# Kernel optimization log

Measured on AMD Instinct MI355X. Metric: run time of the kernel, lower is better.

Reference implementation:

```python
import jax, jax.numpy as jnp
import numpy as np

B, T, E, U, V = 64, 100, 512, 512, 32000


def gru_layer(xs_tm, Wg, bg, Wc, bc):
    """TF GRUCell math. xs_tm: [T, B, D]. Returns (ys [T,B,U], h_final [B,U])."""
    u_dim = Wc.shape[1]
    h0 = jnp.zeros((xs_tm.shape[1], u_dim), xs_tm.dtype)

    def step(h, x):
        ru = jax.nn.sigmoid(jnp.concatenate([x, h], -1) @ Wg + bg)
        r, u = jnp.split(ru, 2, axis=-1)
        c = jnp.tanh(jnp.concatenate([x, r * h], -1) @ Wc + bc)
        h_new = u * h + (1.0 - u) * c
        return h_new, h_new

    h_final, ys = jax.lax.scan(step, h0, xs_tm)
    return ys, h_final


def setup_inputs() -> dict:
    key = jax.random.key(0)
    ks = jax.random.split(key, 16)

    def w(k, shape):
        fan_in = shape[0]
        return jax.random.normal(k, shape, jnp.float32) * (1.0 / np.sqrt(fan_in))

    inp = {
        "x": jax.random.randint(ks[0], (B, T), 0, V, jnp.int32),
        "embedding": jax.random.normal(ks[1], (V, E), jnp.float32) * 0.02,
        # bi-directional layer, input dim E
        "Wg_fw": w(ks[2], (E + U, 2 * U)), "bg_fw": jnp.ones((2 * U,), jnp.float32),
        "Wc_fw": w(ks[3], (E + U, U)),     "bc_fw": jnp.zeros((U,), jnp.float32),
        "Wg_bw": w(ks[4], (E + U, 2 * U)), "bg_bw": jnp.ones((2 * U,), jnp.float32),
        "Wc_bw": w(ks[5], (E + U, U)),     "bc_bw": jnp.zeros((U,), jnp.float32),
        # uni layer 1, input dim 2U (concat fw/bw)
        "Wg_u1": w(ks[6], (2 * U + U, 2 * U)), "bg_u1": jnp.ones((2 * U,), jnp.float32),
        "Wc_u1": w(ks[7], (2 * U + U, U)),     "bc_u1": jnp.zeros((U,), jnp.float32),
        # uni layer 2, input dim U
        "Wg_u2": w(ks[8], (U + U, 2 * U)), "bg_u2": jnp.ones((2 * U,), jnp.float32),
        "Wc_u2": w(ks[9], (U + U, U)),     "bc_u2": jnp.zeros((U,), jnp.float32),
    }
    return inp


def reference(x, embedding, Wg_fw, bg_fw, Wc_fw, bc_fw, Wg_bw, bg_bw, Wc_bw, bc_bw,
              Wg_u1, bg_u1, Wc_u1, bc_u1, Wg_u2, bg_u2, Wc_u2, bc_u2):
    emb = embedding[x]                      # [B, T, E] embedding lookup
    xs = jnp.swapaxes(emb, 0, 1)            # [T, B, E] time-major for scan
    # bidirectional GRU layer
    yf, _ = gru_layer(xs, Wg_fw, bg_fw, Wc_fw, bc_fw)
    yb, _ = gru_layer(xs[::-1], Wg_bw, bg_bw, Wc_bw, bc_bw)
    a = jnp.concatenate([yf, yb[::-1]], -1)  # [T, B, 2U]
    # 2-layer unidirectional GRU stack (MultiRNNCell)
    a, s1 = gru_layer(a, Wg_u1, bg_u1, Wc_u1, bc_u1)
    a, s2 = gru_layer(a, Wg_u2, bg_u2, Wc_u2, bc_u2)
    output = jnp.swapaxes(a, 0, 1)          # [B, T, U]
    state = jnp.stack([s1, s2])             # [2, B, U] per-layer final states
    return output, state
```

## Files before the change

### kernel.cpp

```cpp
#include <hip/hip_runtime.h>
#include <hip/hip_bf16.h>


#define TT 100

using f32x4 = __attribute__((ext_vector_type(4))) float;
using s16x8 = __attribute__((ext_vector_type(8))) short;
using u32x4 = __attribute__((ext_vector_type(4))) unsigned;

__device__ __forceinline__ unsigned short f2bfu(float x) {
  __hip_bfloat16 b = __float2bfloat16(x);
  unsigned short u;
  __builtin_memcpy(&u, &b, sizeof(u));
  return u;
}
__device__ __forceinline__ float bfu2f(unsigned short u) {
  __hip_bfloat16 b;
  __builtin_memcpy(&b, &u, sizeof(b));
  return __bfloat162float(b);
}
__device__ __forceinline__ float sigm(float x) {
  x = fminf(fmaxf(x, -30.f), 30.f);
  return 1.f / (1.f + __expf(-x));
}
__device__ __forceinline__ float tanh_fast(float x) {
  x = fminf(fmaxf(x, -15.f), 15.f);
  float e = __expf(-2.f * x);
  return (1.f - e) / (1.f + e);
}
__device__ __forceinline__ void vm_drain() {
  asm volatile("s_waitcnt vmcnt(0)" ::: "memory");
}
__device__ __forceinline__ void sc1_store_b16(void* p, unsigned v) {
  asm volatile("global_store_short %0, %1, off sc0 sc1" :: "v"(p), "v"(v) : "memory");
}

__global__ __launch_bounds__(256) void pack_w_kernel(const float* __restrict__ Wg,
                                                     const float* __restrict__ Wc,
                                                     int ldg, int ldc, int ktTot,
                                                     unsigned short* __restrict__ hi,
                                                     unsigned short* __restrict__ lo) {
  const int gg = blockIdx.x * 256 + threadIdx.x;
  if (gg >= 96 * ktTot * 64) return;
  const int lane = gg & 63;
  const int pair = gg >> 6;
  const int kt = pair % ktTot;
  const int nt = pair / ktTot;
  const int kg = lane >> 4;
  const int nl = lane & 15;
  const size_t off = (size_t)gg * 8;
  for (int i = 0; i < 8; ++i) {
    const int k = kt * 32 + kg * 8 + i;
    float v = (nt < 64) ? Wg[(size_t)k * ldg + nt * 16 + nl]
                        : Wc[(size_t)k * ldc + (nt - 64) * 16 + nl];
    unsigned short h = f2bfu(v);
    hi[off + i] = h;
    lo[off + i] = f2bfu(v - bfu2f(h));
  }
}

template <int ASRC>
__global__ __launch_bounds__(256) void gemm_mfma(
    const int* __restrict__ xtok, const float* __restrict__ emb,
    const unsigned short* __restrict__ aHi, const unsigned short* __restrict__ aLo, int lda,
    const unsigned short* __restrict__ bHi, const unsigned short* __restrict__ bLo,
    int ktTot, int ktX,
    const float* __restrict__ bg, const float* __restrict__ bc,
    float* __restrict__ C) {
  __shared__ unsigned short Ah[128 * 40];
  __shared__ unsigned short Al[128 * 40];

  const int tid = threadIdx.x;
  const int lane = tid & 63;
  const int w = tid >> 6;
  const int bm = blockIdx.x, bn = blockIdx.y;
  const int fm = lane & 15, fkg = lane >> 4;

  const int arow = tid >> 1;
  const int koff = (tid & 1) * 16;
  const int rowg = bm * 128 + arow;

  f32x4 acc[2][8];
#pragma unroll
  for (int rt = 0; rt < 2; ++rt)
#pragma unroll
    for (int ni = 0; ni < 8; ++ni) acc[rt][ni] = (f32x4){0.f, 0.f, 0.f, 0.f};

  for (int kt = 0; kt < ktX; ++kt) {
    __syncthreads();
    {
      const size_t so = (size_t)rowg * lda + kt * 32 + koff;
      s16x8 h0 = *(const s16x8*)(aHi + so);
      s16x8 h1 = *(const s16x8*)(aHi + so + 8);
      s16x8 l0 = *(const s16x8*)(aLo + so);
      s16x8 l1 = *(const s16x8*)(aLo + so + 8);
      *(s16x8*)(Ah + arow * 40 + koff) = h0;
      *(s16x8*)(Ah + arow * 40 + koff + 8) = h1;
      *(s16x8*)(Al + arow * 40 + koff) = l0;
      *(s16x8*)(Al + arow * 40 + koff + 8) = l1;
    }
    __syncthreads();

    s16x8 ah[2], al[2];
#pragma unroll
    for (int rt = 0; rt < 2; ++rt) {
      const int m = w * 32 + rt * 16 + fm;
      ah[rt] = *(const s16x8*)(Ah + m * 40 + fkg * 8);
      al[rt] = *(const s16x8*)(Al + m * 40 + fkg * 8);
    }
#pragma unroll
    for (int ni = 0; ni < 8; ++ni) {
      const int nt = bn * 8 + ni;
      const size_t bo = ((size_t)nt * ktTot + kt) * 512 + lane * 8;
      s16x8 bh = *(const s16x8*)(bHi + bo);
      s16x8 bl = *(const s16x8*)(bLo + bo);
#pragma unroll
      for (int rt = 0; rt < 2; ++rt) {
        acc[rt][ni] = __builtin_amdgcn_mfma_f32_16x16x32_bf16(ah[rt], bh, acc[rt][ni], 0, 0, 0);
        acc[rt][ni] = __builtin_amdgcn_mfma_f32_16x16x32_bf16(ah[rt], bl, acc[rt][ni], 0, 0, 0);
        acc[rt][ni] = __builtin_amdgcn_mfma_f32_16x16x32_bf16(al[rt], bh, acc[rt][ni], 0, 0, 0);
      }
    }
  }

#pragma unroll
  for (int ni = 0; ni < 8; ++ni) {
    const int nt = bn * 8 + ni;
    int dcol; float bias;
    if (nt < 64) { dcol = nt * 16 + fm; bias = bg[dcol]; }
    else { dcol = 1024 + (nt - 64) * 16 + fm; bias = bc[(nt - 64) * 16 + fm]; }
#pragma unroll
    for (int rt = 0; rt < 2; ++rt)
#pragma unroll
      for (int j = 0; j < 4; ++j) {
        const int row = bm * 128 + w * 32 + rt * 16 + fkg * 4 + j;
        C[(size_t)row * 1536 + dcol] = acc[rt][ni][j] + bias;
      }
  }
}

__global__ __launch_bounds__(256, 1) void bidir_scan_kernel(
    const int* __restrict__ xtok, const float* __restrict__ emb,
    const unsigned short* __restrict__ wHiF, const unsigned short* __restrict__ wLoF,
    const unsigned short* __restrict__ wHiB, const unsigned short* __restrict__ wLoB,
    const float* __restrict__ bgF, const float* __restrict__ bcF,
    const float* __restrict__ bgB, const float* __restrict__ bcB,
    unsigned* __restrict__ hPkG, unsigned* __restrict__ rPkG,
    unsigned* __restrict__ slots,
    unsigned short* __restrict__ yHi, unsigned short* __restrict__ yLo) {
  __shared__ unsigned short wHi_s[3 * 8192];
  __shared__ unsigned short wLo_s[3 * 8192];
  __shared__ float scr[4][16][17];
  __shared__ float scr2[4][16][17];
  __shared__ float scr3[4][16][17];

  const int tid = threadIdx.x;
  const int lane = tid & 63;
  const int wv = tid >> 6;
  const int bid = blockIdx.x;
  const int g = bid & 7;
  const int wg = bid >> 3;
  const int hs = wg << 4;
  const int dir = g & 1;
  const int b0 = (g >> 1) << 4;

  const unsigned short* wph = dir ? wHiB : wHiF;
  const unsigned short* wpl = dir ? wLoB : wLoF;
  const float* bgD = dir ? bgB : bgF;
  const float* bcD = dir ? bcB : bcF;

  {
    const int nt0[3] = {wg, 32 + wg, 64 + wg};
    for (int c = 0; c < 3; ++c) {
      const unsigned short* sH = wph + ((size_t)nt0[c] * 32 + 16) * 512;
      const unsigned short* sL = wpl + ((size_t)nt0[c] * 32 + 16) * 512;
      unsigned short* dH = wHi_s + c * 8192;
      unsigned short* dL = wLo_s + c * 8192;
#pragma unroll
      for (int it = 0; it < 4; ++it) {
        const int o = (it * 256 + tid) * 8;
        *(s16x8*)(dH + o) = *(const s16x8*)(sH + o);
        *(s16x8*)(dL + o) = *(const s16x8*)(sL + o);
      }
    }
  }
  __syncthreads();

  unsigned* gslots = slots + g * 32;
  const int fm = lane & 15;
  const int fkg = lane >> 4;
  const int afe = fm * 512;
  const int asw = (fm & 7) << 3;
  const int ob = tid >> 4, oj = tid & 15;
  const int ui = ob * 512 + ((hs + oj) ^ ((ob & 7) << 3));
  const size_t tileo = (size_t)g * 8192;
  const float br = bgD[hs + oj], bu = bgD[512 + hs + oj], bcv = bcD[hs + oj];

  auto mfma_regs = [&](int cidx, const s16x8* ah, const s16x8* al,
                       float (*dst)[16][17]) {
    f32x4 acc0 = {0.f, 0.f, 0.f, 0.f}, acc1 = {0.f, 0.f, 0.f, 0.f};
#pragma unroll
    for (int q = 0; q < 4; ++q) {
      const int kt = wv * 4 + q;
      const int wo = ((cidx * 16 + kt) * 64 + lane) * 8;
      s16x8 bh = *(const s16x8*)(wHi_s + wo);
      s16x8 bl = *(const s16x8*)(wLo_s + wo);
      if (q & 1) {
        acc1 = __builtin_amdgcn_mfma_f32_16x16x32_bf16(ah[q], bh, acc1, 0, 0, 0);
        acc1 = __builtin_amdgcn_mfma_f32_16x16x32_bf16(ah[q], bl, acc1, 0, 0, 0);
        acc1 = __builtin_amdgcn_mfma_f32_16x16x32_bf16(al[q], bh, acc1, 0, 0, 0);
      } else {
        acc0 = __builtin_amdgcn_mfma_f32_16x16x32_bf16(ah[q], bh, acc0, 0, 0, 0);
        acc0 = __builtin_amdgcn_mfma_f32_16x16x32_bf16(ah[q], bl, acc0, 0, 0, 0);
        acc0 = __builtin_amdgcn_mfma_f32_16x16x32_bf16(al[q], bh, acc0, 0, 0, 0);
      }
    }
#pragma unroll
    for (int j = 0; j < 4; ++j) dst[wv][fkg * 4 + j][fm] = acc0[j] + acc1[j];
  };

  auto mfma_xpg = [&](int nt, const s16x8* xh, const s16x8* xl,
                      float (*dst)[16][17]) {
    f32x4 acc0 = {0.f, 0.f, 0.f, 0.f}, acc1 = {0.f, 0.f, 0.f, 0.f};
#pragma unroll
    for (int q = 0; q < 4; ++q) {
      const int kt = wv * 4 + q;
      const size_t bo = ((size_t)nt * 32 + kt) * 512 + lane * 8;
      s16x8 bh = *(const s16x8*)(wph + bo);
      s16x8 bl = *(const s16x8*)(wpl + bo);
      if (q & 1) {
        acc1 = __builtin_amdgcn_mfma_f32_16x16x32_bf16(xh[q], bh, acc1, 0, 0, 0);
        acc1 = __builtin_amdgcn_mfma_f32_16x16x32_bf16(xh[q], bl, acc1, 0, 0, 0);
        acc1 = __builtin_amdgcn_mfma_f32_16x16x32_bf16(xl[q], bh, acc1, 0, 0, 0);
      } else {
        acc0 = __builtin_amdgcn_mfma_f32_16x16x32_bf16(xh[q], bh, acc0, 0, 0, 0);
        acc0 = __builtin_amdgcn_mfma_f32_16x16x32_bf16(xh[q], bl, acc0, 0, 0, 0);
        acc0 = __builtin_amdgcn_mfma_f32_16x16x32_bf16(xl[q], bh, acc0, 0, 0, 0);
      }
    }
#pragma unroll
    for (int j = 0; j < 4; ++j) dst[wv][fkg * 4 + j][fm] = acc0[j] + acc1[j];
  };

  auto load_emb_frags = [&](int tg, s16x8* xh, s16x8* xl) {
    const int tok = xtok[(b0 + fm) * TT + tg];
    const float* er = emb + (size_t)tok * 512;
#pragma unroll
    for (int q = 0; q < 4; ++q) {
      const int kt = wv * 4 + q;
      const float* p = er + kt * 32 + fkg * 8;
      f32x4 a = *(const f32x4*)p;
      f32x4 b = *(const f32x4*)(p + 4);
      s16x8 hh, ll;
#pragma unroll
      for (int j = 0; j < 4; ++j) {
        unsigned short h1 = f2bfu(a[j]);
        hh[j] = (short)h1; ll[j] = (short)f2bfu(a[j] - bfu2f(h1));
        unsigned short h2 = f2bfu(b[j]);
        hh[j + 4] = (short)h2; ll[j + 4] = (short)f2bfu(b[j] - bfu2f(h2));
      }
      xh[q] = hh; xl[q] = ll;
    }
  };

  auto load_frags = [&](const unsigned* pk, s16x8* ah, s16x8* al,
                        bool withHv, unsigned* hvOut) {
    u32x4 d[4][2];
#pragma unroll
    for (int q = 0; q < 4; ++q) {
      const int kt = wv * 4 + q;
      const unsigned* p = pk + tileo + afe + ((kt * 32 + fkg * 8) ^ asw);
      asm volatile("global_load_dwordx4 %0, %1, off sc0 sc1"
                   : "=v"(d[q][0]) : "v"(p) : "memory");
      asm volatile("global_load_dwordx4 %0, %1, off sc0 sc1"
                   : "=v"(d[q][1]) : "v"(p + 4) : "memory");
    }
    if (withHv)
      asm volatile("global_load_dword %0, %1, off sc0 sc1"
                   : "=v"(*hvOut) : "v"(pk + tileo + ui) : "memory");
    vm_drain();
    __builtin_amdgcn_sched_barrier(0);
#pragma unroll
    for (int q = 0; q < 4; ++q) {
      u32x4 hh, ll;
#pragma unroll
      for (int i = 0; i < 2; ++i) {
        const u32x4 dd = d[q][i];
        hh[2 * i] = (dd[0] & 0xffffu) | (dd[1] << 16);
        hh[2 * i + 1] = (dd[2] & 0xffffu) | (dd[3] << 16);
        ll[2 * i] = (dd[0] >> 16) | (dd[1] & 0xffff0000u);
        ll[2 * i + 1] = (dd[2] >> 16) | (dd[3] & 0xffff0000u);
      }
      __builtin_memcpy(&ah[q], &hh, 16);
      __builtin_memcpy(&al[q], &ll, 16);
    }
  };

  auto poll = [&](unsigned target) {
    if (tid < 32) {
      const unsigned* p = gslots + tid;
      unsigned v;
      do {
        asm volatile("global_load_dword %0, %1, off sc0 sc1\n\ts_waitcnt vmcnt(0)"
                     : "=v"(v) : "v"(p) : "memory");
      } while (!__all(v >= target));
    }
    __syncthreads();
  };

  float gxr, gxu, gxc;
  {
    s16x8 xh0[4], xl0[4];
    load_emb_frags(dir ? TT - 1 : 0, xh0, xl0);
    mfma_xpg(wg, xh0, xl0, scr);
    mfma_xpg(32 + wg, xh0, xl0, scr2);
    mfma_xpg(64 + wg, xh0, xl0, scr3);
    __syncthreads();
    gxr = scr[0][ob][oj] + scr[1][ob][oj] + scr[2][ob][oj] + scr[3][ob][oj] + br;
    gxu = scr2[0][ob][oj] + scr2[1][ob][oj] + scr2[2][ob][oj] + scr2[3][ob][oj] + bu;
    gxc = scr3[0][ob][oj] + scr3[1][ob][oj] + scr3[2][ob][oj] + scr3[3][ob][oj] + bcv;
    __syncthreads();
  }

  s16x8 xh[4], xl[4];
  for (int t = 0; t < TT; ++t) {
    const int tg = dir ? (TT - 1 - t) : t;

    s16x8 ah[4], al[4];
    unsigned hvu = 0;
    load_frags(hPkG, ah, al, true, &hvu);
    mfma_regs(0, ah, al, scr);
    __syncthreads();

    float rpre = scr[0][ob][oj] + scr[1][ob][oj] + scr[2][ob][oj] + scr[3][ob][oj] + gxr;
    float sg = sigm(rpre);
    float hv = bfu2f((unsigned short)(hvu & 0xffffu)) + bfu2f((unsigned short)(hvu >> 16));
    float rh = sg * hv;
    {
      unsigned short hh_ = f2bfu(rh);
      unsigned short ll_ = f2bfu(rh - bfu2f(hh_));
      unsigned e = (unsigned)hh_ | ((unsigned)ll_ << 16);
      asm volatile("global_store_dword %0, %1, off sc0 sc1"
                   :: "v"(rPkG + tileo + ui), "v"(e) : "memory");
    }
    vm_drain();
    __syncthreads();
    if (tid == 0) {
      unsigned tv = 2 * t + 1;
      asm volatile("global_store_dword %0, %1, off sc0 sc1"
                   :: "v"(gslots + wg), "v"(tv) : "memory");
    }

    mfma_regs(1, ah, al, scr2);
    float ngxr = 0.f, ngxu = 0.f, ngxc = 0.f;
    if (t + 1 < TT) {
      load_emb_frags(dir ? TT - 2 - t : t + 1, xh, xl);
      mfma_xpg(32 + wg, xh, xl, scr);
      mfma_xpg(64 + wg, xh, xl, scr3);
      __syncthreads();
      ngxu = scr[0][ob][oj] + scr[1][ob][oj] + scr[2][ob][oj] + scr[3][ob][oj] + bu;
      ngxc = scr3[0][ob][oj] + scr3[1][ob][oj] + scr3[2][ob][oj] + scr3[3][ob][oj] + bcv;
      __syncthreads();
    }

    poll(2 * t + 1);

    load_frags(rPkG, ah, al, false, nullptr);
    mfma_regs(2, ah, al, scr);
    __syncthreads();

    float upre = scr2[0][ob][oj] + scr2[1][ob][oj] + scr2[2][ob][oj] + scr2[3][ob][oj] + gxu;
    float uv = sigm(upre);
    float cpre = scr[0][ob][oj] + scr[1][ob][oj] + scr[2][ob][oj] + scr[3][ob][oj] + gxc;
    float hn = uv * hv + (1.f - uv) * tanh_fast(cpre);
    unsigned short hh_ = f2bfu(hn);
    unsigned short ll_ = f2bfu(hn - bfu2f(hh_));

    if (t == TT - 1) {
      const size_t yi = ((size_t)tg * 64 + (b0 + ob)) * 1024 + dir * 512 + hs + oj;
      yHi[yi] = hh_; yLo[yi] = ll_;
      break;
    }

    {
      unsigned e = (unsigned)hh_ | ((unsigned)ll_ << 16);
      asm volatile("global_store_dword %0, %1, off sc0 sc1"
                   :: "v"(hPkG + tileo + ui), "v"(e) : "memory");
    }
    vm_drain();
    __syncthreads();
    if (tid == 0) {
      unsigned tv = 2 * t + 2;
      asm volatile("global_store_dword %0, %1, off sc0 sc1"
                   :: "v"(gslots + wg), "v"(tv) : "memory");
    }

    {
      const size_t yi = ((size_t)tg * 64 + (b0 + ob)) * 1024 + dir * 512 + hs + oj;
      yHi[yi] = hh_; yLo[yi] = ll_;
    }
    {
      mfma_xpg(wg, xh, xl, scr);
      __syncthreads();
      ngxr = scr[0][ob][oj] + scr[1][ob][oj] + scr[2][ob][oj] + scr[3][ob][oj] + br;
    }
    gxr = ngxr; gxu = ngxu; gxc = ngxc;

    poll(2 * t + 2);
  }
}

__global__ __launch_bounds__(256, 1) void uni_fused_kernel(
    const float* __restrict__ gx1,
    const unsigned short* __restrict__ w1Hi, const unsigned short* __restrict__ w1Lo,
    const unsigned short* __restrict__ w2Hi, const unsigned short* __restrict__ w2Lo,
    const float* __restrict__ bg2, const float* __restrict__ bc2,
    unsigned* __restrict__ hPk1, unsigned* __restrict__ rPk1,
    unsigned* __restrict__ hPk2, unsigned* __restrict__ rPk2,
    unsigned* __restrict__ slots1, unsigned* __restrict__ slots2,
    unsigned short* __restrict__ y1Hi, unsigned short* __restrict__ y1Lo,
    float* __restrict__ out, float* __restrict__ st1, float* __restrict__ st2) {
  __shared__ unsigned short wHi_s[3 * 8192];
  __shared__ unsigned short wLo_s[3 * 8192];
  __shared__ float scr[4][16][17];
  __shared__ float scr2[4][16][17];
  __shared__ float scr3[4][16][17];

  const int tid = threadIdx.x;
  const int lane = tid & 63;
  const int wv = tid >> 6;
  const int bid = blockIdx.x;
  const int role = (bid >= 128);
  const int g = (bid & 127) >> 5;
  const int wg = bid & 31;
  const int hs = wg << 4;
  const int b0 = g * 16;

  const unsigned short* wph = role ? w2Hi : w1Hi;
  const unsigned short* wpl = role ? w2Lo : w1Lo;
  const int ktTot = role ? 32 : 48;
  const int ktH0 = role ? 16 : 32;
  unsigned* hPk = role ? hPk2 : hPk1;
  unsigned* rPk = role ? rPk2 : rPk1;
  unsigned* myslots = (role ? slots2 : slots1) + g * 32;
  unsigned* u1gs = slots1 + g * 32;

  {
    const int nt0[3] = {wg, 32 + wg, 64 + wg};
    for (int c = 0; c < 3; ++c) {
      const unsigned short* sH = wph + ((size_t)nt0[c] * ktTot + ktH0) * 512;
      const unsigned short* sL = wpl + ((size_t)nt0[c] * ktTot + ktH0) * 512;
      unsigned short* dH = wHi_s + c * 8192;
      unsigned short* dL = wLo_s + c * 8192;
#pragma unroll
      for (int it = 0; it < 4; ++it) {
        const int o = (it * 256 + tid) * 8;
        *(s16x8*)(dH + o) = *(const s16x8*)(sH + o);
        *(s16x8*)(dL + o) = *(const s16x8*)(sL + o);
      }
    }
  }
  __syncthreads();

  const int fm = lane & 15;
  const int fkg = lane >> 4;
  const int afe = fm * 512;
  const int asw = (fm & 7) << 3;
  const int ob = tid >> 4, oj = tid & 15;
  const int ui = ob * 512 + ((hs + oj) ^ ((ob & 7) << 3));
  const size_t tileo = (size_t)g * 8192;

  auto mfma_regs = [&](int cidx, const s16x8* ah, const s16x8* al,
                       float (*dst)[16][17]) {
    f32x4 acc0 = {0.f, 0.f, 0.f, 0.f}, acc1 = {0.f, 0.f, 0.f, 0.f};
#pragma unroll
    for (int q = 0; q < 4; ++q) {
      const int kt = wv * 4 + q;
      const int wo = ((cidx * 16 + kt) * 64 + lane) * 8;
      s16x8 bh = *(const s16x8*)(wHi_s + wo);
      s16x8 bl = *(const s16x8*)(wLo_s + wo);
      if (q & 1) {
        acc1 = __builtin_amdgcn_mfma_f32_16x16x32_bf16(ah[q], bh, acc1, 0, 0, 0);
        acc1 = __builtin_amdgcn_mfma_f32_16x16x32_bf16(ah[q], bl, acc1, 0, 0, 0);
        acc1 = __builtin_amdgcn_mfma_f32_16x16x32_bf16(al[q], bh, acc1, 0, 0, 0);
      } else {
        acc0 = __builtin_amdgcn_mfma_f32_16x16x32_bf16(ah[q], bh, acc0, 0, 0, 0);
        acc0 = __builtin_amdgcn_mfma_f32_16x16x32_bf16(ah[q], bl, acc0, 0, 0, 0);
        acc0 = __builtin_amdgcn_mfma_f32_16x16x32_bf16(al[q], bh, acc0, 0, 0, 0);
      }
    }
#pragma unroll
    for (int j = 0; j < 4; ++j) dst[wv][fkg * 4 + j][fm] = acc0[j] + acc1[j];
  };

  auto mfma_xp = [&](int cidx, const s16x8* xh, const s16x8* xl,
                     float (*dst)[16][17]) {
    const int nt0[3] = {wg, 32 + wg, 64 + wg};
    f32x4 acc0 = {0.f, 0.f, 0.f, 0.f}, acc1 = {0.f, 0.f, 0.f, 0.f};
#pragma unroll
    for (int q = 0; q < 4; ++q) {
      const int kt = wv * 4 + q;
      const size_t bo = ((size_t)nt0[cidx] * 32 + kt) * 512 + lane * 8;
      s16x8 bh = *(const s16x8*)(w2Hi + bo);
      s16x8 bl = *(const s16x8*)(w2Lo + bo);
      if (q & 1) {
        acc1 = __builtin_amdgcn_mfma_f32_16x16x32_bf16(xh[q], bh, acc1, 0, 0, 0);
        acc1 = __builtin_amdgcn_mfma_f32_16x16x32_bf16(xh[q], bl, acc1, 0, 0, 0);
        acc1 = __builtin_amdgcn_mfma_f32_16x16x32_bf16(xl[q], bh, acc1, 0, 0, 0);
      } else {
        acc0 = __builtin_amdgcn_mfma_f32_16x16x32_bf16(xh[q], bh, acc0, 0, 0, 0);
        acc0 = __builtin_amdgcn_mfma_f32_16x16x32_bf16(xh[q], bl, acc0, 0, 0, 0);
        acc0 = __builtin_amdgcn_mfma_f32_16x16x32_bf16(xl[q], bh, acc0, 0, 0, 0);
      }
    }
#pragma unroll
    for (int j = 0; j < 4; ++j) dst[wv][fkg * 4 + j][fm] = acc0[j] + acc1[j];
  };

  auto load_y1_frags = [&](int t_, s16x8* xh, s16x8* xl) {
#pragma unroll
    for (int q = 0; q < 4; ++q) {
      const int kt = wv * 4 + q;
      const size_t yo = ((size_t)t_ * 64 + b0 + fm) * 512 + kt * 32 + fkg * 8;
      asm volatile("global_load_dwordx4 %0, %1, off sc0 sc1"
                   : "=v"(xh[q]) : "v"(y1Hi + yo) : "memory");
      asm volatile("global_load_dwordx4 %0, %1, off sc0 sc1"
                   : "=v"(xl[q]) : "v"(y1Lo + yo) : "memory");
    }
    vm_drain();
    __builtin_amdgcn_sched_barrier(0);
  };

  auto load_frags = [&](const unsigned* pk, s16x8* ah, s16x8* al,
                        bool withHv, unsigned* hvOut) {
    u32x4 d[4][2];
#pragma unroll
    for (int q = 0; q < 4; ++q) {
      const int kt = wv * 4 + q;
      const unsigned* p = pk + tileo + afe + ((kt * 32 + fkg * 8) ^ asw);
      asm volatile("global_load_dwordx4 %0, %1, off sc0 sc1"
                   : "=v"(d[q][0]) : "v"(p) : "memory");
      asm volatile("global_load_dwordx4 %0, %1, off sc0 sc1"
                   : "=v"(d[q][1]) : "v"(p + 4) : "memory");
    }
    if (withHv)
      asm volatile("global_load_dword %0, %1, off sc0 sc1"
                   : "=v"(*hvOut) : "v"(pk + tileo + ui) : "memory");
    vm_drain();
    __builtin_amdgcn_sched_barrier(0);
#pragma unroll
    for (int q = 0; q < 4; ++q) {
      u32x4 hh, ll;
#pragma unroll
      for (int i = 0; i < 2; ++i) {
        const u32x4 dd = d[q][i];
        hh[2 * i] = (dd[0] & 0xffffu) | (dd[1] << 16);
        hh[2 * i + 1] = (dd[2] & 0xffffu) | (dd[3] << 16);
        ll[2 * i] = (dd[0] >> 16) | (dd[1] & 0xffff0000u);
        ll[2 * i + 1] = (dd[2] >> 16) | (dd[3] & 0xffff0000u);
      }
      __builtin_memcpy(&ah[q], &hh, 16);
      __builtin_memcpy(&al[q], &ll, 16);
    }
  };

  auto poll_arr = [&](const unsigned* arr, unsigned target) {
    if (tid < 32) {
      const unsigned* p = arr + tid;
      unsigned v;
      do {
        asm volatile("global_load_dword %0, %1, off sc0 sc1\n\ts_waitcnt vmcnt(0)"
                     : "=v"(v) : "v"(p) : "memory");
      } while (!__all(v >= target));
    }
    __syncthreads();
  };

  if (role == 0) {
    float gxr, gxu, gxc;
    {
      const float* row = gx1 + ((size_t)0 * 64 + b0 + ob) * 1536 + hs + oj;
      gxr = row[0]; gxu = row[512]; gxc = row[1024];
    }
    for (int t = 0; t < TT; ++t) {
      s16x8 ah[4], al[4];
      unsigned hvu = 0;
      load_frags(hPk, ah, al, true, &hvu);
      mfma_regs(0, ah, al, scr);
      __syncthreads();

      float rpre = scr[0][ob][oj] + scr[1][ob][oj] + scr[2][ob][oj] + scr[3][ob][oj] + gxr;
      float sg = sigm(rpre);
      float hv = bfu2f((unsigned short)(hvu & 0xffffu)) + bfu2f((unsigned short)(hvu >> 16));
      float rh = sg * hv;
      {
        unsigned short hh_ = f2bfu(rh);
        unsigned short ll_ = f2bfu(rh - bfu2f(hh_));
        unsigned e = (unsigned)hh_ | ((unsigned)ll_ << 16);
        asm volatile("global_store_dword %0, %1, off sc0 sc1"
                     :: "v"(rPk + tileo + ui), "v"(e) : "memory");
      }
      vm_drain();
      __syncthreads();
      if (tid == 0) {
        unsigned tv = 2 * t + 1;
        asm volatile("global_store_dword %0, %1, off sc0 sc1"
                     :: "v"(myslots + wg), "v"(tv) : "memory");
      }

      mfma_regs(1, ah, al, scr2);

      float ngxr = 0.f, ngxu = 0.f, ngxc = 0.f;
      if (t + 1 < TT) {
        const float* row = gx1 + ((size_t)(t + 1) * 64 + b0 + ob) * 1536 + hs + oj;
        ngxr = row[0]; ngxu = row[512]; ngxc = row[1024];
      }

      poll_arr(myslots, 2 * t + 1);

      load_frags(rPk, ah, al, false, nullptr);
      mfma_regs(2, ah, al, scr);
      __syncthreads();

      float upre = scr2[0][ob][oj] + scr2[1][ob][oj] + scr2[2][ob][oj] + scr2[3][ob][oj] + gxu;
      float uv = sigm(upre);
      float cpre = scr[0][ob][oj] + scr[1][ob][oj] + scr[2][ob][oj] + scr[3][ob][oj] + gxc;
      float hn = uv * hv + (1.f - uv) * tanh_fast(cpre);
      unsigned short hh_ = f2bfu(hn);
      unsigned short ll_ = f2bfu(hn - bfu2f(hh_));

      {
        const size_t yi = ((size_t)t * 64 + (b0 + ob)) * 512 + hs + oj;
        sc1_store_b16(y1Hi + yi, hh_);
        sc1_store_b16(y1Lo + yi, ll_);
      }
      if (t < TT - 1) {
        unsigned e = (unsigned)hh_ | ((unsigned)ll_ << 16);
        asm volatile("global_store_dword %0, %1, off sc0 sc1"
                     :: "v"(hPk + tileo + ui), "v"(e) : "memory");
      } else {
        st1[(size_t)(b0 + ob) * 512 + hs + oj] = hn;
      }
      vm_drain();
      __syncthreads();
      if (tid == 0) {
        unsigned tv = 2 * t + 2;
        asm volatile("global_store_dword %0, %1, off sc0 sc1"
                     :: "v"(myslots + wg), "v"(tv) : "memory");
      }
      if (t == TT - 1) break;
      gxr = ngxr; gxu = ngxu; gxc = ngxc;
      poll_arr(myslots, 2 * t + 2);
    }
  } else {
    const float br = bg2[hs + oj], bu = bg2[512 + hs + oj], bc_ = bc2[hs + oj];
    s16x8 xh[4], xl[4];
    float gxr, gxu, gxc;
    {
      poll_arr(u1gs, 2);
      load_y1_frags(0, xh, xl);
      mfma_xp(0, xh, xl, scr);
      mfma_xp(1, xh, xl, scr2);
      mfma_xp(2, xh, xl, scr3);
      __syncthreads();
      gxr = scr[0][ob][oj] + scr[1][ob][oj] + scr[2][ob][oj] + scr[3][ob][oj] + br;
      gxu = scr2[0][ob][oj] + scr2[1][ob][oj] + scr2[2][ob][oj] + scr2[3][ob][oj] + bu;
      gxc = scr3[0][ob][oj] + scr3[1][ob][oj] + scr3[2][ob][oj] + scr3[3][ob][oj] + bc_;
      __syncthreads();
    }
    for (int t = 0; t < TT; ++t) {
      s16x8 ah[4], al[4];
      unsigned hvu = 0;
      load_frags(hPk, ah, al, true, &hvu);
      mfma_regs(0, ah, al, scr);
      __syncthreads();

      float rpre = scr[0][ob][oj] + scr[1][ob][oj] + scr[2][ob][oj] + scr[3][ob][oj] + gxr;
      float sg = sigm(rpre);
      float hv = bfu2f((unsigned short)(hvu & 0xffffu)) + bfu2f((unsigned short)(hvu >> 16));
      float rh = sg * hv;
      {
        unsigned short hh_ = f2bfu(rh);
        unsigned short ll_ = f2bfu(rh - bfu2f(hh_));
        unsigned e = (unsigned)hh_ | ((unsigned)ll_ << 16);
        asm volatile("global_store_dword %0, %1, off sc0 sc1"
                     :: "v"(rPk + tileo + ui), "v"(e) : "memory");
      }
      vm_drain();
      __syncthreads();
      if (tid == 0) {
        unsigned tv = 2 * t + 1;
        asm volatile("global_store_dword %0, %1, off sc0 sc1"
                     :: "v"(myslots + wg), "v"(tv) : "memory");
      }

      mfma_regs(1, ah, al, scr2);
      float ngxr = 0.f, ngxu = 0.f, ngxc = 0.f;
      if (t + 1 < TT) {
        poll_arr(u1gs, 2 * (t + 1) + 2);
        load_y1_frags(t + 1, xh, xl);
        mfma_xp(1, xh, xl, scr);
        mfma_xp(2, xh, xl, scr3);
        __syncthreads();
        ngxu = scr[0][ob][oj] + scr[1][ob][oj] + scr[2][ob][oj] + scr[3][ob][oj] + bu;
        ngxc = scr3[0][ob][oj] + scr3[1][ob][oj] + scr3[2][ob][oj] + scr3[3][ob][oj] + bc_;
        __syncthreads();
      }

      poll_arr(myslots, 2 * t + 1);

      load_frags(rPk, ah, al, false, nullptr);
      mfma_regs(2, ah, al, scr);
      __syncthreads();

      float upre = scr2[0][ob][oj] + scr2[1][ob][oj] + scr2[2][ob][oj] + scr2[3][ob][oj] + gxu;
      float uv = sigm(upre);
      float cpre = scr[0][ob][oj] + scr[1][ob][oj] + scr[2][ob][oj] + scr[3][ob][oj] + gxc;
      float hn = uv * hv + (1.f - uv) * tanh_fast(cpre);

      if (t == TT - 1) {
        out[((size_t)(b0 + ob) * TT + t) * 512 + hs + oj] = hn;
        st2[(size_t)(b0 + ob) * 512 + hs + oj] = hn;
        break;
      }
      {
        unsigned short hh_ = f2bfu(hn);
        unsigned short ll_ = f2bfu(hn - bfu2f(hh_));
        unsigned e = (unsigned)hh_ | ((unsigned)ll_ << 16);
        asm volatile("global_store_dword %0, %1, off sc0 sc1"
                     :: "v"(hPk + tileo + ui), "v"(e) : "memory");
      }
      vm_drain();
      __syncthreads();
      if (tid == 0) {
        unsigned tv = 2 * t + 2;
        asm volatile("global_store_dword %0, %1, off sc0 sc1"
                     :: "v"(myslots + wg), "v"(tv) : "memory");
      }

      out[((size_t)(b0 + ob) * TT + t) * 512 + hs + oj] = hn;
      {
        mfma_xp(0, xh, xl, scr);
        __syncthreads();
        ngxr = scr[0][ob][oj] + scr[1][ob][oj] + scr[2][ob][oj] + scr[3][ob][oj] + br;
      }
      gxr = ngxr; gxu = ngxu; gxc = ngxc;
      poll_arr(myslots, 2 * t + 2);
    }
  }
}

extern "C" void kernel_launch(void* const* d_in, const int* in_sizes, int n_in,
                              void* d_out, int out_size, void* d_ws, size_t ws_size,
                              hipStream_t stream) {
  (void)in_sizes; (void)n_in; (void)out_size; (void)ws_size;
  const int* x = (const int*)d_in[0];
  const float* emb = (const float*)d_in[1];
  const float* WgFw = (const float*)d_in[2];
  const float* bgFw = (const float*)d_in[3];
  const float* WcFw = (const float*)d_in[4];
  const float* bcFw = (const float*)d_in[5];
  const float* WgBw = (const float*)d_in[6];
  const float* bgBw = (const float*)d_in[7];
  const float* WcBw = (const float*)d_in[8];
  const float* bcBw = (const float*)d_in[9];
  const float* WgU1 = (const float*)d_in[10];
  const float* bgU1 = (const float*)d_in[11];
  const float* WcU1 = (const float*)d_in[12];
  const float* bcU1 = (const float*)d_in[13];
  const float* WgU2 = (const float*)d_in[14];
  const float* bgU2 = (const float*)d_in[15];
  const float* WcU2 = (const float*)d_in[16];
  const float* bcU2 = (const float*)d_in[17];

  char* ws = (char*)d_ws;
  float* bufA = (float*)(ws + 0);
  unsigned short* ycatHi = (unsigned short*)(ws + 78643200);
  unsigned short* ycatLo = (unsigned short*)(ws + 91750400);
  unsigned short* y1Hi = (unsigned short*)(ws + 78643200);
  unsigned short* y1Lo = (unsigned short*)(ws + 85196800);
  unsigned short* wpFwHi = (unsigned short*)(ws + 104857600);
  unsigned short* wpFwLo = (unsigned short*)(ws + 108003328);
  unsigned short* wpBwHi = (unsigned short*)(ws + 111149056);
  unsigned short* wpBwLo = (unsigned short*)(ws + 114294784);
  unsigned short* wpU1Hi = (unsigned short*)(ws + 117440512);
  unsigned short* wpU1Lo = (unsigned short*)(ws + 122159104);
  unsigned short* wpU2Hi = (unsigned short*)(ws + 104857600);
  unsigned short* wpU2Lo = (unsigned short*)(ws + 108003328);
  unsigned* tiles = (unsigned*)(ws + 126877696);
  unsigned* bars = (unsigned*)(ws + 127401984);

  unsigned* hPkB = tiles;
  unsigned* rPkB = tiles + 65536;
  unsigned* hPk1 = tiles;
  unsigned* rPk1 = tiles + 32768;
  unsigned* hPk2 = tiles + 65536;
  unsigned* rPk2 = tiles + 98304;

  float* out = (float*)d_out;
  float* st1 = out + (size_t)64 * TT * 512;
  float* st2 = st1 + 64 * 512;

  hipMemsetAsync(bars, 0, 4096, stream);

  pack_w_kernel<<<768, 256, 0, stream>>>(WgFw, WcFw, 1024, 512, 32, wpFwHi, wpFwLo);
  pack_w_kernel<<<768, 256, 0, stream>>>(WgBw, WcBw, 1024, 512, 32, wpBwHi, wpBwLo);
  pack_w_kernel<<<1152, 256, 0, stream>>>(WgU1, WcU1, 1024, 512, 48, wpU1Hi, wpU1Lo);

  hipMemsetAsync(tiles, 0, 524288, stream);
  {
    const int* xt = x;
    const float* em = emb;
    const unsigned short *w0 = wpFwHi, *w1 = wpFwLo, *w2 = wpBwHi, *w3 = wpBwLo;
    const float *bF = bgFw, *cF = bcFw, *bB = bgBw, *cB = bcBw;
    unsigned *h0 = hPkB, *r0 = rPkB;
    unsigned* bp = bars;
    unsigned short *yh = ycatHi, *yl = ycatLo;
    void* args[] = {&xt, &em, &w0, &w1, &w2, &w3, &bF, &cF, &bB, &cB,
                    &h0, &r0, &bp, &yh, &yl};
    hipLaunchCooperativeKernel((const void*)bidir_scan_kernel, dim3(256), dim3(256),
                               args, 0, stream);
  }

  pack_w_kernel<<<768, 256, 0, stream>>>(WgU2, WcU2, 1024, 512, 32, wpU2Hi, wpU2Lo);

  gemm_mfma<1><<<dim3(50, 12), 256, 0, stream>>>(
      nullptr, nullptr, ycatHi, ycatLo, 1024, wpU1Hi, wpU1Lo, 48, 32, bgU1, bcU1, bufA);

  hipMemsetAsync(tiles, 0, 524288, stream);
  {
    const float* a0 = bufA;
    const unsigned short *w0 = wpU1Hi, *w1 = wpU1Lo, *w2 = wpU2Hi, *w3 = wpU2Lo;
    const float *b2 = bgU2, *c2 = bcU2;
    unsigned *h1 = hPk1, *r1 = rPk1, *h2 = hPk2, *r2 = rPk2;
    unsigned *s1p = bars + 256, *s2p = bars + 384;
    unsigned short *yh = y1Hi, *yl = y1Lo;
    float *op = out, *t1 = st1, *t2 = st2;
    void* args[] = {&a0, &w0, &w1, &w2, &w3, &b2, &c2,
                    &h1, &r1, &h2, &r2, &s1p, &s2p, &yh, &yl, &op, &t1, &t2};
    hipLaunchCooperativeKernel((const void*)uni_fused_kernel, dim3(256), dim3(256),
                               args, 0, stream);
  }
}
```

Baseline: 1.555 ms.

## Replace slot-counter barriers with tagged data records and double-buffered state tiles

Inter-block synchronization in the recurrent scan kernels no longer uses per-group counter slots with drain, syncthreads and polling. Each hidden-state and r*h value is now stored as a 64-bit record carrying its timestep tag, and consumers spin until every record they load has the expected tag. The h tiles are double-buffered by timestep parity so writers never overwrite data still being read. The goal is to remove the store-drain, flag-write and poll round trips from the critical path of each step. The cost is doubled payload traffic for state loads, a larger memset including a 26 MB y1 record buffer, and retry loads when data is not yet ready.

```diff
diff --git a/kernel.cpp b/kernel.cpp
--- a/kernel.cpp
+++ b/kernel.cpp
@@ -6,7 +6,11 @@
 
 using f32x4 = __attribute__((ext_vector_type(4))) float;
 using s16x8 = __attribute__((ext_vector_type(8))) short;
+using u32x2 = __attribute__((ext_vector_type(2))) unsigned;
 using u32x4 = __attribute__((ext_vector_type(4))) unsigned;
+typedef unsigned long long u64;
+
+#define PARSTRIDE 65536
 
 __device__ __forceinline__ unsigned short f2bfu(float x) {
   __hip_bfloat16 b = __float2bfloat16(x);
@@ -31,8 +35,9 @@
 __device__ __forceinline__ void vm_drain() {
   asm volatile("s_waitcnt vmcnt(0)" ::: "memory");
 }
-__device__ __forceinline__ void sc1_store_b16(void* p, unsigned v) {
-  asm volatile("global_store_short %0, %1, off sc0 sc1" :: "v"(p), "v"(v) : "memory");
+__device__ __forceinline__ void rec_store(u64* p, unsigned val, unsigned tag) {
+  u32x2 e; e[0] = val; e[1] = tag;
+  asm volatile("global_store_dwordx2 %0, %1, off sc0 sc1" :: "v"(p), "v"(e) : "memory");
 }
 
 __global__ __launch_bounds__(256) void pack_w_kernel(const float* __restrict__ Wg,
@@ -59,9 +64,7 @@
   }
 }
 
-template <int ASRC>
 __global__ __launch_bounds__(256) void gemm_mfma(
-    const int* __restrict__ xtok, const float* __restrict__ emb,
     const unsigned short* __restrict__ aHi, const unsigned short* __restrict__ aLo, int lda,
     const unsigned short* __restrict__ bHi, const unsigned short* __restrict__ bLo,
     int ktTot, int ktX,
@@ -145,14 +148,16 @@
     const unsigned short* __restrict__ wHiB, const unsigned short* __restrict__ wLoB,
     const float* __restrict__ bgF, const float* __restrict__ bcF,
     const float* __restrict__ bgB, const float* __restrict__ bcB,
-    unsigned* __restrict__ hPkG, unsigned* __restrict__ rPkG,
-    unsigned* __restrict__ slots,
+    u64* __restrict__ hT0, u64* __restrict__ rT0,
     unsigned short* __restrict__ yHi, unsigned short* __restrict__ yLo) {
   __shared__ unsigned short wHi_s[3 * 8192];
   __shared__ unsigned short wLo_s[3 * 8192];
-  __shared__ float scr[4][16][17];
-  __shared__ float scr2[4][16][17];
-  __shared__ float scr3[4][16][17];
+  __shared__ float scrR[4][16][17];
+  __shared__ float scrU[4][16][17];
+  __shared__ float scrC[4][16][17];
+  __shared__ float scrXU[4][16][17];
+  __shared__ float scrXC[4][16][17];
+  __shared__ float scrXR[4][16][17];
 
   const int tid = threadIdx.x;
   const int lane = tid & 63;
@@ -186,7 +191,6 @@
   }
   __syncthreads();
 
-  unsigned* gslots = slots + g * 32;
   const int fm = lane & 15;
   const int fkg = lane >> 4;
   const int afe = fm * 512;
@@ -263,150 +267,125 @@
     }
   };
 
-  auto load_frags = [&](const unsigned* pk, s16x8* ah, s16x8* al,
-                        bool withHv, unsigned* hvOut) {
-    u32x4 d[4][2];
+  auto load_frags_tag = [&](const u64* pkt, unsigned tag, s16x8* ah, s16x8* al,
+                            bool withHv, unsigned* hvOut) {
+    u32x4 d[4][4];
+    u32x2 hv2 = {0, 0};
+    while (true) {
+#pragma unroll
+      for (int q = 0; q < 4; ++q) {
+        const int kt = wv * 4 + q;
+        const unsigned* p = (const unsigned*)(pkt + tileo + afe + ((kt * 32 + fkg * 8) ^ asw));
+#pragma unroll
+        for (int i = 0; i < 4; ++i)
+          asm volatile("global_load_dwordx4 %0, %1, off sc0 sc1"
+                       : "=v"(d[q][i]) : "v"(p + 4 * i) : "memory");
+      }
+      if (withHv)
+        asm volatile("global_load_dwordx2 %0, %1, off sc0 sc1"
+                     : "=v"(hv2) : "v"((const unsigned*)(pkt + tileo + ui)) : "memory");
+      vm_drain();
+      __builtin_amdgcn_sched_barrier(0);
+      bool ok = true;
+#pragma unroll
+      for (int q = 0; q < 4; ++q)
+#pragma unroll
+        for (int i = 0; i < 4; ++i) ok &= (d[q][i][1] == tag) & (d[q][i][3] == tag);
+      if (withHv) ok &= (hv2[1] == tag);
+      if (__all(ok)) break;
+      __builtin_amdgcn_s_sleep(1);
+    }
+    if (withHv) *hvOut = hv2[0];
 #pragma unroll
     for (int q = 0; q < 4; ++q) {
-      const int kt = wv * 4 + q;
-      const unsigned* p = pk + tileo + afe + ((kt * 32 + fkg * 8) ^ asw);
-      asm volatile("global_load_dwordx4 %0, %1, off sc0 sc1"
-                   : "=v"(d[q][0]) : "v"(p) : "memory");
-      asm volatile("global_load_dwordx4 %0, %1, off sc0 sc1"
-                   : "=v"(d[q][1]) : "v"(p + 4) : "memory");
-    }
-    if (withHv)
-      asm volatile("global_load_dword %0, %1, off sc0 sc1"
-                   : "=v"(*hvOut) : "v"(pk + tileo + ui) : "memory");
-    vm_drain();
-    __builtin_amdgcn_sched_barrier(0);
-#pragma unroll
-    for (int q = 0; q < 4; ++q) {
+      unsigned val[8];
+#pragma unroll
+      for (int j = 0; j < 8; ++j) val[j] = d[q][j >> 1][(j & 1) * 2];
       u32x4 hh, ll;
 #pragma unroll
-      for (int i = 0; i < 2; ++i) {
-        const u32x4 dd = d[q][i];
-        hh[2 * i] = (dd[0] & 0xffffu) | (dd[1] << 16);
-        hh[2 * i + 1] = (dd[2] & 0xffffu) | (dd[3] << 16);
-        ll[2 * i] = (dd[0] >> 16) | (dd[1] & 0xffff0000u);
-        ll[2 * i + 1] = (dd[2] >> 16) | (dd[3] & 0xffff0000u);
+      for (int k = 0; k < 4; ++k) {
+        const unsigned v0 = val[2 * k], v1 = val[2 * k + 1];
+        hh[k] = (v0 & 0xffffu) | (v1 << 16);
+        ll[k] = (v0 >> 16) | (v1 & 0xffff0000u);
       }
       __builtin_memcpy(&ah[q], &hh, 16);
       __builtin_memcpy(&al[q], &ll, 16);
     }
-  };
-
-  auto poll = [&](unsigned target) {
-    if (tid < 32) {
-      const unsigned* p = gslots + tid;
-      unsigned v;
-      do {
-        asm volatile("global_load_dword %0, %1, off sc0 sc1\n\ts_waitcnt vmcnt(0)"
-                     : "=v"(v) : "v"(p) : "memory");
-      } while (!__all(v >= target));
-    }
-    __syncthreads();
   };
 
   float gxr, gxu, gxc;
   {
     s16x8 xh0[4], xl0[4];
     load_emb_frags(dir ? TT - 1 : 0, xh0, xl0);
-    mfma_xpg(wg, xh0, xl0, scr);
-    mfma_xpg(32 + wg, xh0, xl0, scr2);
-    mfma_xpg(64 + wg, xh0, xl0, scr3);
-    __syncthreads();
-    gxr = scr[0][ob][oj] + scr[1][ob][oj] + scr[2][ob][oj] + scr[3][ob][oj] + br;
-    gxu = scr2[0][ob][oj] + scr2[1][ob][oj] + scr2[2][ob][oj] + scr2[3][ob][oj] + bu;
-    gxc = scr3[0][ob][oj] + scr3[1][ob][oj] + scr3[2][ob][oj] + scr3[3][ob][oj] + bcv;
+    mfma_xpg(wg, xh0, xl0, scrR);
+    mfma_xpg(32 + wg, xh0, xl0, scrU);
+    mfma_xpg(64 + wg, xh0, xl0, scrC);
+    __syncthreads();
+    gxr = scrR[0][ob][oj] + scrR[1][ob][oj] + scrR[2][ob][oj] + scrR[3][ob][oj] + br;
+    gxu = scrU[0][ob][oj] + scrU[1][ob][oj] + scrU[2][ob][oj] + scrU[3][ob][oj] + bu;
+    gxc = scrC[0][ob][oj] + scrC[1][ob][oj] + scrC[2][ob][oj] + scrC[3][ob][oj] + bcv;
     __syncthreads();
   }
 
   s16x8 xh[4], xl[4];
   for (int t = 0; t < TT; ++t) {
     const int tg = dir ? (TT - 1 - t) : t;
+    u64* hTc = hT0 + (size_t)(t & 1) * PARSTRIDE;
+    u64* hTn = hT0 + (size_t)((t + 1) & 1) * PARSTRIDE;
+    u64* rTc = rT0 + (size_t)(t & 1) * PARSTRIDE;
 
     s16x8 ah[4], al[4];
     unsigned hvu = 0;
-    load_frags(hPkG, ah, al, true, &hvu);
-    mfma_regs(0, ah, al, scr);
-    __syncthreads();
-
-    float rpre = scr[0][ob][oj] + scr[1][ob][oj] + scr[2][ob][oj] + scr[3][ob][oj] + gxr;
+    load_frags_tag(hTc, (unsigned)t, ah, al, true, &hvu);
+    mfma_regs(0, ah, al, scrR);
+    __syncthreads();
+
+    float rpre = scrR[0][ob][oj] + scrR[1][ob][oj] + scrR[2][ob][oj] + scrR[3][ob][oj] + gxr;
     float sg = sigm(rpre);
     float hv = bfu2f((unsigned short)(hvu & 0xffffu)) + bfu2f((unsigned short)(hvu >> 16));
     float rh = sg * hv;
     {
       unsigned short hh_ = f2bfu(rh);
       unsigned short ll_ = f2bfu(rh - bfu2f(hh_));
-      unsigned e = (unsigned)hh_ | ((unsigned)ll_ << 16);
-      asm volatile("global_store_dword %0, %1, off sc0 sc1"
-                   :: "v"(rPkG + tileo + ui), "v"(e) : "memory");
-    }
-    vm_drain();
-    __syncthreads();
-    if (tid == 0) {
-      unsigned tv = 2 * t + 1;
-      asm volatile("global_store_dword %0, %1, off sc0 sc1"
-                   :: "v"(gslots + wg), "v"(tv) : "memory");
-    }
-
-    mfma_regs(1, ah, al, scr2);
+      rec_store(rTc + tileo + ui, (unsigned)hh_ | ((unsigned)ll_ << 16), (unsigned)(t + 1));
+    }
+
+    mfma_regs(1, ah, al, scrU);
     float ngxr = 0.f, ngxu = 0.f, ngxc = 0.f;
     if (t + 1 < TT) {
       load_emb_frags(dir ? TT - 2 - t : t + 1, xh, xl);
-      mfma_xpg(32 + wg, xh, xl, scr);
-      mfma_xpg(64 + wg, xh, xl, scr3);
-      __syncthreads();
-      ngxu = scr[0][ob][oj] + scr[1][ob][oj] + scr[2][ob][oj] + scr[3][ob][oj] + bu;
-      ngxc = scr3[0][ob][oj] + scr3[1][ob][oj] + scr3[2][ob][oj] + scr3[3][ob][oj] + bcv;
-      __syncthreads();
-    }
-
-    poll(2 * t + 1);
-
-    load_frags(rPkG, ah, al, false, nullptr);
-    mfma_regs(2, ah, al, scr);
-    __syncthreads();
-
-    float upre = scr2[0][ob][oj] + scr2[1][ob][oj] + scr2[2][ob][oj] + scr2[3][ob][oj] + gxu;
+      mfma_xpg(32 + wg, xh, xl, scrXU);
+      mfma_xpg(64 + wg, xh, xl, scrXC);
+    }
+    __syncthreads();
+    if (t + 1 < TT) {
+      ngxu = scrXU[0][ob][oj] + scrXU[1][ob][oj] + scrXU[2][ob][oj] + scrXU[3][ob][oj] + bu;
+      ngxc = scrXC[0][ob][oj] + scrXC[1][ob][oj] + scrXC[2][ob][oj] + scrXC[3][ob][oj] + bcv;
+    }
+
+    load_frags_tag(rTc, (unsigned)(t + 1), ah, al, false, nullptr);
+    mfma_regs(2, ah, al, scrC);
+    __syncthreads();
+
+    float upre = scrU[0][ob][oj] + scrU[1][ob][oj] + scrU[2][ob][oj] + scrU[3][ob][oj] + gxu;
     float uv = sigm(upre);
-    float cpre = scr[0][ob][oj] + scr[1][ob][oj] + scr[2][ob][oj] + scr[3][ob][oj] + gxc;
+    float cpre = scrC[0][ob][oj] + scrC[1][ob][oj] + scrC[2][ob][oj] + scrC[3][ob][oj] + gxc;
     float hn = uv * hv + (1.f - uv) * tanh_fast(cpre);
     unsigned short hh_ = f2bfu(hn);
     unsigned short ll_ = f2bfu(hn - bfu2f(hh_));
 
-    if (t == TT - 1) {
-      const size_t yi = ((size_t)tg * 64 + (b0 + ob)) * 1024 + dir * 512 + hs + oj;
-      yHi[yi] = hh_; yLo[yi] = ll_;
-      break;
-    }
-
-    {
-      unsigned e = (unsigned)hh_ | ((unsigned)ll_ << 16);
-      asm volatile("global_store_dword %0, %1, off sc0 sc1"
-                   :: "v"(hPkG + tileo + ui), "v"(e) : "memory");
-    }
-    vm_drain();
-    __syncthreads();
-    if (tid == 0) {
-      unsigned tv = 2 * t + 2;
-      asm volatile("global_store_dword %0, %1, off sc0 sc1"
-                   :: "v"(gslots + wg), "v"(tv) : "memory");
-    }
-
     {
       const size_t yi = ((size_t)tg * 64 + (b0 + ob)) * 1024 + dir * 512 + hs + oj;
       yHi[yi] = hh_; yLo[yi] = ll_;
     }
-    {
-      mfma_xpg(wg, xh, xl, scr);
-      __syncthreads();
-      ngxr = scr[0][ob][oj] + scr[1][ob][oj] + scr[2][ob][oj] + scr[3][ob][oj] + br;
-    }
+    if (t == TT - 1) break;
+    rec_store(hTn + tileo + ui, (unsigned)hh_ | ((unsigned)ll_ << 16), (unsigned)(t + 1));
+
+    mfma_xpg(wg, xh, xl, scrXR);
+    __syncthreads();
+    ngxr = scrXR[0][ob][oj] + scrXR[1][ob][oj] + scrXR[2][ob][oj] + scrXR[3][ob][oj] + br;
     gxr = ngxr; gxu = ngxu; gxc = ngxc;
-
-    poll(2 * t + 2);
+    __syncthreads();
   }
 }
 
@@ -415,16 +394,17 @@
     const unsigned short* __restrict__ w1Hi, const unsigned short* __restrict__ w1Lo,
     const unsigned short* __restrict__ w2Hi, const unsigned short* __restrict__ w2Lo,
     const float* __restrict__ bg2, const float* __restrict__ bc2,
-    unsigned* __restrict__ hPk1, unsigned* __restrict__ rPk1,
-    unsigned* __restrict__ hPk2, unsigned* __restrict__ rPk2,
-    unsigned* __restrict__ slots1, unsigned* __restrict__ slots2,
-    unsigned short* __restrict__ y1Hi, unsigned short* __restrict__ y1Lo,
+    u64* __restrict__ hT0, u64* __restrict__ rT0,
+    u64* __restrict__ y1rec,
     float* __restrict__ out, float* __restrict__ st1, float* __restrict__ st2) {
   __shared__ unsigned short wHi_s[3 * 8192];
   __shared__ unsigned short wLo_s[3 * 8192];
-  __shared__ float scr[4][16][17];
-  __shared__ float scr2[4][16][17];
-  __shared__ float scr3[4][16][17];
+  __shared__ float scrR[4][16][17];
+  __shared__ float scrU[4][16][17];
+  __shared__ float scrC[4][16][17];
+  __shared__ float scrXU[4][16][17];
+  __shared__ float scrXC[4][16][17];
+  __shared__ float scrXR[4][16][17];
 
   const int tid = threadIdx.x;
   const int lane = tid & 63;
@@ -440,10 +420,6 @@
   const unsigned short* wpl = role ? w2Lo : w1Lo;
   const int ktTot = role ? 32 : 48;
   const int ktH0 = role ? 16 : 32;
-  unsigned* hPk = role ? hPk2 : hPk1;
-  unsigned* rPk = role ? rPk2 : rPk1;
-  unsigned* myslots = (role ? slots2 : slots1) + g * 32;
-  unsigned* u1gs = slots1 + g * 32;
 
   {
     const int nt0[3] = {wg, 32 + wg, 64 + wg};
@@ -468,7 +444,7 @@
   const int asw = (fm & 7) << 3;
   const int ob = tid >> 4, oj = tid & 15;
   const int ui = ob * 512 + ((hs + oj) ^ ((ob & 7) << 3));
-  const size_t tileo = (size_t)g * 8192;
+  const size_t tileo = (size_t)(role * 4 + g) * 8192;
 
   auto mfma_regs = [&](int cidx, const s16x8* ah, const s16x8* al,
                        float (*dst)[16][17]) {
@@ -517,63 +493,90 @@
     for (int j = 0; j < 4; ++j) dst[wv][fkg * 4 + j][fm] = acc0[j] + acc1[j];
   };
 
-  auto load_y1_frags = [&](int t_, s16x8* xh, s16x8* xl) {
+  auto load_frags_tag = [&](const u64* pkt, unsigned tag, s16x8* ah, s16x8* al,
+                            bool withHv, unsigned* hvOut) {
+    u32x4 d[4][4];
+    u32x2 hv2 = {0, 0};
+    while (true) {
+#pragma unroll
+      for (int q = 0; q < 4; ++q) {
+        const int kt = wv * 4 + q;
+        const unsigned* p = (const unsigned*)(pkt + tileo + afe + ((kt * 32 + fkg * 8) ^ asw));
+#pragma unroll
+        for (int i = 0; i < 4; ++i)
+          asm volatile("global_load_dwordx4 %0, %1, off sc0 sc1"
+                       : "=v"(d[q][i]) : "v"(p + 4 * i) : "memory");
+      }
+      if (withHv)
+        asm volatile("global_load_dwordx2 %0, %1, off sc0 sc1"
+                     : "=v"(hv2) : "v"((const unsigned*)(pkt + tileo + ui)) : "memory");
+      vm_drain();
+      __builtin_amdgcn_sched_barrier(0);
+      bool ok = true;
+#pragma unroll
+      for (int q = 0; q < 4; ++q)
+#pragma unroll
+        for (int i = 0; i < 4; ++i) ok &= (d[q][i][1] == tag) & (d[q][i][3] == tag);
+      if (withHv) ok &= (hv2[1] == tag);
+      if (__all(ok)) break;
+      __builtin_amdgcn_s_sleep(1);
+    }
+    if (withHv) *hvOut = hv2[0];
 #pragma unroll
     for (int q = 0; q < 4; ++q) {
-      const int kt = wv * 4 + q;
-      const size_t yo = ((size_t)t_ * 64 + b0 + fm) * 512 + kt * 32 + fkg * 8;
-      asm volatile("global_load_dwordx4 %0, %1, off sc0 sc1"
-                   : "=v"(xh[q]) : "v"(y1Hi + yo) : "memory");
-      asm volatile("global_load_dwordx4 %0, %1, off sc0 sc1"
-                   : "=v"(xl[q]) : "v"(y1Lo + yo) : "memory");
-    }
-    vm_drain();
-    __builtin_amdgcn_sched_barrier(0);
-  };
-
-  auto load_frags = [&](const unsigned* pk, s16x8* ah, s16x8* al,
-                        bool withHv, unsigned* hvOut) {
-    u32x4 d[4][2];
-#pragma unroll
-    for (int q = 0; q < 4; ++q) {
-      const int kt = wv * 4 + q;
-      const unsigned* p = pk + tileo + afe + ((kt * 32 + fkg * 8) ^ asw);
-      asm volatile("global_load_dwordx4 %0, %1, off sc0 sc1"
-                   : "=v"(d[q][0]) : "v"(p) : "memory");
-      asm volatile("global_load_dwordx4 %0, %1, off sc0 sc1"
-                   : "=v"(d[q][1]) : "v"(p + 4) : "memory");
-    }
-    if (withHv)
-      asm volatile("global_load_dword %0, %1, off sc0 sc1"
-                   : "=v"(*hvOut) : "v"(pk + tileo + ui) : "memory");
-    vm_drain();
-    __builtin_amdgcn_sched_barrier(0);
-#pragma unroll
-    for (int q = 0; q < 4; ++q) {
+      unsigned val[8];
+#pragma unroll
+      for (int j = 0; j < 8; ++j) val[j] = d[q][j >> 1][(j & 1) * 2];
       u32x4 hh, ll;
 #pragma unroll
-      for (int i = 0; i < 2; ++i) {
-        const u32x4 dd = d[q][i];
-        hh[2 * i] = (dd[0] & 0xffffu) | (dd[1] << 16);
-        hh[2 * i + 1] = (dd[2] & 0xffffu) | (dd[3] << 16);
-        ll[2 * i] = (dd[0] >> 16) | (dd[1] & 0xffff0000u);
-        ll[2 * i + 1] = (dd[2] >> 16) | (dd[3] & 0xffff0000u);
+      for (int k = 0; k < 4; ++k) {
+        const unsigned v0 = val[2 * k], v1 = val[2 * k + 1];
+        hh[k] = (v0 & 0xffffu) | (v1 << 16);
+        ll[k] = (v0 >> 16) | (v1 & 0xffff0000u);
       }
       __builtin_memcpy(&ah[q], &hh, 16);
       __builtin_memcpy(&al[q], &ll, 16);
     }
   };
 
-  auto poll_arr = [&](const unsigned* arr, unsigned target) {
-    if (tid < 32) {
-      const unsigned* p = arr + tid;
-      unsigned v;
-      do {
-        asm volatile("global_load_dword %0, %1, off sc0 sc1\n\ts_waitcnt vmcnt(0)"
-                     : "=v"(v) : "v"(p) : "memory");
-      } while (!__all(v >= target));
-    }
-    __syncthreads();
+  auto load_y1_tag = [&](int t_, s16x8* xh, s16x8* xl) {
+    const unsigned tag = (unsigned)(t_ + 1);
+    u32x4 d[4][4];
+    while (true) {
+#pragma unroll
+      for (int q = 0; q < 4; ++q) {
+        const int kt = wv * 4 + q;
+        const unsigned* p = (const unsigned*)(y1rec + ((size_t)t_ * 64 + b0 + fm) * 512 + kt * 32 + fkg * 8);
+#pragma unroll
+        for (int i = 0; i < 4; ++i)
+          asm volatile("global_load_dwordx4 %0, %1, off sc0 sc1"
+                       : "=v"(d[q][i]) : "v"(p + 4 * i) : "memory");
+      }
+      vm_drain();
+      __builtin_amdgcn_sched_barrier(0);
+      bool ok = true;
+#pragma unroll
+      for (int q = 0; q < 4; ++q)
+#pragma unroll
+        for (int i = 0; i < 4; ++i) ok &= (d[q][i][1] == tag) & (d[q][i][3] == tag);
+      if (__all(ok)) break;
+      __builtin_amdgcn_s_sleep(1);
+    }
+#pragma unroll
+    for (int q = 0; q < 4; ++q) {
+      unsigned val[8];
+#pragma unroll
+      for (int j = 0; j < 8; ++j) val[j] = d[q][j >> 1][(j & 1) * 2];
+      u32x4 hh, ll;
+#pragma unroll
+      for (int k = 0; k < 4; ++k) {
+        const unsigned v0 = val[2 * k], v1 = val[2 * k + 1];
+        hh[k] = (v0 & 0xffffu) | (v1 << 16);
+        ll[k] = (v0 >> 16) | (v1 & 0xffff0000u);
+      }
+      __builtin_memcpy(&xh[q], &hh, 16);
+      __builtin_memcpy(&xl[q], &ll, 16);
+    }
   };
 
   if (role == 0) {
@@ -583,169 +586,128 @@
       gxr = row[0]; gxu = row[512]; gxc = row[1024];
     }
     for (int t = 0; t < TT; ++t) {
+      u64* hTc = hT0 + (size_t)(t & 1) * PARSTRIDE;
+      u64* hTn = hT0 + (size_t)((t + 1) & 1) * PARSTRIDE;
+      u64* rTc = rT0 + (size_t)(t & 1) * PARSTRIDE;
+
       s16x8 ah[4], al[4];
       unsigned hvu = 0;
-      load_frags(hPk, ah, al, true, &hvu);
-      mfma_regs(0, ah, al, scr);
-      __syncthreads();
-
-      float rpre = scr[0][ob][oj] + scr[1][ob][oj] + scr[2][ob][oj] + scr[3][ob][oj] + gxr;
+      load_frags_tag(hTc, (unsigned)t, ah, al, true, &hvu);
+      mfma_regs(0, ah, al, scrR);
+      __syncthreads();
+
+      float rpre = scrR[0][ob][oj] + scrR[1][ob][oj] + scrR[2][ob][oj] + scrR[3][ob][oj] + gxr;
       float sg = sigm(rpre);
       float hv = bfu2f((unsigned short)(hvu & 0xffffu)) + bfu2f((unsigned short)(hvu >> 16));
       float rh = sg * hv;
       {
         unsigned short hh_ = f2bfu(rh);
         unsigned short ll_ = f2bfu(rh - bfu2f(hh_));
-        unsigned e = (unsigned)hh_ | ((unsigned)ll_ << 16);
-        asm volatile("global_store_dword %0, %1, off sc0 sc1"
-                     :: "v"(rPk + tileo + ui), "v"(e) : "memory");
-      }
-      vm_drain();
-      __syncthreads();
-      if (tid == 0) {
-        unsigned tv = 2 * t + 1;
-        asm volatile("global_store_dword %0, %1, off sc0 sc1"
-                     :: "v"(myslots + wg), "v"(tv) : "memory");
-      }
-
-      mfma_regs(1, ah, al, scr2);
-
+        rec_store(rTc + tileo + ui, (unsigned)hh_ | ((unsigned)ll_ << 16), (unsigned)(t + 1));
+      }
+
+      mfma_regs(1, ah, al, scrU);
       float ngxr = 0.f, ngxu = 0.f, ngxc = 0.f;
       if (t + 1 < TT) {
         const float* row = gx1 + ((size_t)(t + 1) * 64 + b0 + ob) * 1536 + hs + oj;
         ngxr = row[0]; ngxu = row[512]; ngxc = row[1024];
       }
 
-      poll_arr(myslots, 2 * t + 1);
-
-      load_frags(rPk, ah, al, false, nullptr);
-      mfma_regs(2, ah, al, scr);
-      __syncthreads();
-
-      float upre = scr2[0][ob][oj] + scr2[1][ob][oj] + scr2[2][ob][oj] + scr2[3][ob][oj] + gxu;
+      load_frags_tag(rTc, (unsigned)(t + 1), ah, al, false, nullptr);
+      mfma_regs(2, ah, al, scrC);
+      __syncthreads();
+
+      float upre = scrU[0][ob][oj] + scrU[1][ob][oj] + scrU[2][ob][oj] + scrU[3][ob][oj] + gxu;
       float uv = sigm(upre);
-      float cpre = scr[0][ob][oj] + scr[1][ob][oj] + scr[2][ob][oj] + scr[3][ob][oj] + gxc;
+      float cpre = scrC[0][ob][oj] + scrC[1][ob][oj] + scrC[2][ob][oj] + scrC[3][ob][oj] + gxc;
       float hn = uv * hv + (1.f - uv) * tanh_fast(cpre);
       unsigned short hh_ = f2bfu(hn);
       unsigned short ll_ = f2bfu(hn - bfu2f(hh_));
 
-      {
-        const size_t yi = ((size_t)t * 64 + (b0 + ob)) * 512 + hs + oj;
-        sc1_store_b16(y1Hi + yi, hh_);
-        sc1_store_b16(y1Lo + yi, ll_);
-      }
-      if (t < TT - 1) {
-        unsigned e = (unsigned)hh_ | ((unsigned)ll_ << 16);
-        asm volatile("global_store_dword %0, %1, off sc0 sc1"
-                     :: "v"(hPk + tileo + ui), "v"(e) : "memory");
-      } else {
+      rec_store(y1rec + ((size_t)t * 64 + (b0 + ob)) * 512 + hs + oj,
+                (unsigned)hh_ | ((unsigned)ll_ << 16), (unsigned)(t + 1));
+      if (t == TT - 1) {
         st1[(size_t)(b0 + ob) * 512 + hs + oj] = hn;
-      }
-      vm_drain();
-      __syncthreads();
-      if (tid == 0) {
-        unsigned tv = 2 * t + 2;
-        asm volatile("global_store_dword %0, %1, off sc0 sc1"
-                     :: "v"(myslots + wg), "v"(tv) : "memory");
-      }
-      if (t == TT - 1) break;
+        break;
+      }
+      rec_store(hTn + tileo + ui, (unsigned)hh_ | ((unsigned)ll_ << 16), (unsigned)(t + 1));
       gxr = ngxr; gxu = ngxu; gxc = ngxc;
-      poll_arr(myslots, 2 * t + 2);
+      __syncthreads();
     }
   } else {
     const float br = bg2[hs + oj], bu = bg2[512 + hs + oj], bc_ = bc2[hs + oj];
     s16x8 xh[4], xl[4];
     float gxr, gxu, gxc;
     {
-      poll_arr(u1gs, 2);
-      load_y1_frags(0, xh, xl);
-      mfma_xp(0, xh, xl, scr);
-      mfma_xp(1, xh, xl, scr2);
-      mfma_xp(2, xh, xl, scr3);
-      __syncthreads();
-      gxr = scr[0][ob][oj] + scr[1][ob][oj] + scr[2][ob][oj] + scr[3][ob][oj] + br;
-      gxu = scr2[0][ob][oj] + scr2[1][ob][oj] + scr2[2][ob][oj] + scr2[3][ob][oj] + bu;
-      gxc = scr3[0][ob][oj] + scr3[1][ob][oj] + scr3[2][ob][oj] + scr3[3][ob][oj] + bc_;
+      load_y1_tag(0, xh, xl);
+      mfma_xp(0, xh, xl, scrR);
+      mfma_xp(1, xh, xl, scrU);
+      mfma_xp(2, xh, xl, scrC);
+      __syncthreads();
+      gxr = scrR[0][ob][oj] + scrR[1][ob][oj] + scrR[2][ob][oj] + scrR[3][ob][oj] + br;
+      gxu = scrU[0][ob][oj] + scrU[1][ob][oj] + scrU[2][ob][oj] + scrU[3][ob][oj] + bu;
+      gxc = scrC[0][ob][oj] + scrC[1][ob][oj] + scrC[2][ob][oj] + scrC[3][ob][oj] + bc_;
       __syncthreads();
     }
     for (int t = 0; t < TT; ++t) {
+      u64* hTc = hT0 + (size_t)(t & 1) * PARSTRIDE;
+      u64* hTn = hT0 + (size_t)((t + 1) & 1) * PARSTRIDE;
+      u64* rTc = rT0 + (size_t)(t & 1) * PARSTRIDE;
+
       s16x8 ah[4], al[4];
       unsigned hvu = 0;
-      load_frags(hPk, ah, al, true, &hvu);
-      mfma_regs(0, ah, al, scr);
-      __syncthreads();
-
-      float rpre = scr[0][ob][oj] + scr[1][ob][oj] + scr[2][ob][oj] + scr[3][ob][oj] + gxr;
+      load_frags_tag(hTc, (unsigned)t, ah, al, true, &hvu);
+      mfma_regs(0, ah, al, scrR);
+      __syncthreads();
+
+      float rpre = scrR[0][ob][oj] + scrR[1][ob][oj] + scrR[2][ob][oj] + scrR[3][ob][oj] + gxr;
       float sg = sigm(rpre);
       float hv = bfu2f((unsigned short)(hvu & 0xffffu)) + bfu2f((unsigned short)(hvu >> 16));
       float rh = sg * hv;
       {
         unsigned short hh_ = f2bfu(rh);
         unsigned short ll_ = f2bfu(rh - bfu2f(hh_));
-        unsigned e = (unsigned)hh_ | ((unsigned)ll_ << 16);
-        asm volatile("global_store_dword %0, %1, off sc0 sc1"
-                     :: "v"(rPk + tileo + ui), "v"(e) : "memory");
-      }
-      vm_drain();
-      __syncthreads();
-      if (tid == 0) {
-        unsigned tv = 2 * t + 1;
-        asm volatile("global_store_dword %0, %1, off sc0 sc1"
-                     :: "v"(myslots + wg), "v"(tv) : "memory");
-      }
-
-      mfma_regs(1, ah, al, scr2);
+        rec_store(rTc + tileo + ui, (unsigned)hh_ | ((unsigned)ll_ << 16), (unsigned)(t + 1));
+      }
+
+      mfma_regs(1, ah, al, scrU);
       float ngxr = 0.f, ngxu = 0.f, ngxc = 0.f;
       if (t + 1 < TT) {
-        poll_arr(u1gs, 2 * (t + 1) + 2);
-        load_y1_frags(t + 1, xh, xl);
-        mfma_xp(1, xh, xl, scr);
-        mfma_xp(2, xh, xl, scr3);
-        __syncthreads();
-        ngxu = scr[0][ob][oj] + scr[1][ob][oj] + scr[2][ob][oj] + scr[3][ob][oj] + bu;
-        ngxc = scr3[0][ob][oj] + scr3[1][ob][oj] + scr3[2][ob][oj] + scr3[3][ob][oj] + bc_;
-        __syncthreads();
-      }
-
-      poll_arr(myslots, 2 * t + 1);
-
-      load_frags(rPk, ah, al, false, nullptr);
-      mfma_regs(2, ah, al, scr);
-      __syncthreads();
-
-      float upre = scr2[0][ob][oj] + scr2[1][ob][oj] + scr2[2][ob][oj] + scr2[3][ob][oj] + gxu;
+        load_y1_tag(t + 1, xh, xl);
+        mfma_xp(1, xh, xl, scrXU);
+        mfma_xp(2, xh, xl, scrXC);
+      }
+      __syncthreads();
+      if (t + 1 < TT) {
+        ngxu = scrXU[0][ob][oj] + scrXU[1][ob][oj] + scrXU[2][ob][oj] + scrXU[3][ob][oj] + bu;
+        ngxc = scrXC[0][ob][oj] + scrXC[1][ob][oj] + scrXC[2][ob][oj] + scrXC[3][ob][oj] + bc_;
+      }
+
+      load_frags_tag(rTc, (unsigned)(t + 1), ah, al, false, nullptr);
+      mfma_regs(2, ah, al, scrC);
+      __syncthreads();
+
+      float upre = scrU[0][ob][oj] + scrU[1][ob][oj] + scrU[2][ob][oj] + scrU[3][ob][oj] + gxu;
       float uv = sigm(upre);
-      float cpre = scr[0][ob][oj] + scr[1][ob][oj] + scr[2][ob][oj] + scr[3][ob][oj] + gxc;
+      float cpre = scrC[0][ob][oj] + scrC[1][ob][oj] + scrC[2][ob][oj] + scrC[3][ob][oj] + gxc;
       float hn = uv * hv + (1.f - uv) * tanh_fast(cpre);
 
+      out[((size_t)(b0 + ob) * TT + t) * 512 + hs + oj] = hn;
       if (t == TT - 1) {
-        out[((size_t)(b0 + ob) * TT + t) * 512 + hs + oj] = hn;
         st2[(size_t)(b0 + ob) * 512 + hs + oj] = hn;
         break;
       }
       {
         unsigned short hh_ = f2bfu(hn);
         unsigned short ll_ = f2bfu(hn - bfu2f(hh_));
-        unsigned e = (unsigned)hh_ | ((unsigned)ll_ << 16);
-        asm volatile("global_store_dword %0, %1, off sc0 sc1"
-                     :: "v"(hPk + tileo + ui), "v"(e) : "memory");
-      }
-      vm_drain();
-      __syncthreads();
-      if (tid == 0) {
-        unsigned tv = 2 * t + 2;
-        asm volatile("global_store_dword %0, %1, off sc0 sc1"
-                     :: "v"(myslots + wg), "v"(tv) : "memory");
-      }
-
-      out[((size_t)(b0 + ob) * TT + t) * 512 + hs + oj] = hn;
-      {
-        mfma_xp(0, xh, xl, scr);
-        __syncthreads();
-        ngxr = scr[0][ob][oj] + scr[1][ob][oj] + scr[2][ob][oj] + scr[3][ob][oj] + br;
-      }
+        rec_store(hTn + tileo + ui, (unsigned)hh_ | ((unsigned)ll_ << 16), (unsigned)(t + 1));
+      }
+
+      mfma_xp(0, xh, xl, scrXR);
+      __syncthreads();
+      ngxr = scrXR[0][ob][oj] + scrXR[1][ob][oj] + scrXR[2][ob][oj] + scrXR[3][ob][oj] + br;
       gxr = ngxr; gxu = ngxu; gxc = ngxc;
-      poll_arr(myslots, 2 * t + 2);
+      __syncthreads();
     }
   }
 }
@@ -777,8 +739,7 @@
   float* bufA = (float*)(ws + 0);
   unsigned short* ycatHi = (unsigned short*)(ws + 78643200);
   unsigned short* ycatLo = (unsigned short*)(ws + 91750400);
-  unsigned short* y1Hi = (unsigned short*)(ws + 78643200);
-  unsigned short* y1Lo = (unsigned short*)(ws + 85196800);
+  u64* y1rec = (u64*)(ws + 78643200);
   unsigned short* wpFwHi = (unsigned short*)(ws + 104857600);
   unsigned short* wpFwLo = (unsigned short*)(ws + 108003328);
   unsigned short* wpBwHi = (unsigned short*)(ws + 111149056);
@@ -787,57 +748,46 @@
   unsigned short* wpU1Lo = (unsigned short*)(ws + 122159104);
   unsigned short* wpU2Hi = (unsigned short*)(ws + 104857600);
   unsigned short* wpU2Lo = (unsigned short*)(ws + 108003328);
-  unsigned* tiles = (unsigned*)(ws + 126877696);
-  unsigned* bars = (unsigned*)(ws + 127401984);
-
-  unsigned* hPkB = tiles;
-  unsigned* rPkB = tiles + 65536;
-  unsigned* hPk1 = tiles;
-  unsigned* rPk1 = tiles + 32768;
-  unsigned* hPk2 = tiles + 65536;
-  unsigned* rPk2 = tiles + 98304;
+  u64* tiles = (u64*)(ws + 126877696);
+  u64* hT0 = tiles;
+  u64* rT0 = tiles + 131072;
 
   float* out = (float*)d_out;
   float* st1 = out + (size_t)64 * TT * 512;
   float* st2 = st1 + 64 * 512;
 
-  hipMemsetAsync(bars, 0, 4096, stream);
-
   pack_w_kernel<<<768, 256, 0, stream>>>(WgFw, WcFw, 1024, 512, 32, wpFwHi, wpFwLo);
   pack_w_kernel<<<768, 256, 0, stream>>>(WgBw, WcBw, 1024, 512, 32, wpBwHi, wpBwLo);
   pack_w_kernel<<<1152, 256, 0, stream>>>(WgU1, WcU1, 1024, 512, 48, wpU1Hi, wpU1Lo);
 
-  hipMemsetAsync(tiles, 0, 524288, stream);
+  hipMemsetAsync(tiles, 0, 2097152, stream);
   {
     const int* xt = x;
     const float* em = emb;
     const unsigned short *w0 = wpFwHi, *w1 = wpFwLo, *w2 = wpBwHi, *w3 = wpBwLo;
     const float *bF = bgFw, *cF = bcFw, *bB = bgBw, *cB = bcBw;
-    unsigned *h0 = hPkB, *r0 = rPkB;
-    unsigned* bp = bars;
+    u64 *h0 = hT0, *r0 = rT0;
     unsigned short *yh = ycatHi, *yl = ycatLo;
     void* args[] = {&xt, &em, &w0, &w1, &w2, &w3, &bF, &cF, &bB, &cB,
-                    &h0, &r0, &bp, &yh, &yl};
+                    &h0, &r0, &yh, &yl};
     hipLaunchCooperativeKernel((const void*)bidir_scan_kernel, dim3(256), dim3(256),
                                args, 0, stream);
   }
 
   pack_w_kernel<<<768, 256, 0, stream>>>(WgU2, WcU2, 1024, 512, 32, wpU2Hi, wpU2Lo);
 
-  gemm_mfma<1><<<dim3(50, 12), 256, 0, stream>>>(
-      nullptr, nullptr, ycatHi, ycatLo, 1024, wpU1Hi, wpU1Lo, 48, 32, bgU1, bcU1, bufA);
-
-  hipMemsetAsync(tiles, 0, 524288, stream);
+  gemm_mfma<<<dim3(50, 12), 256, 0, stream>>>(
+      ycatHi, ycatLo, 1024, wpU1Hi, wpU1Lo, 48, 32, bgU1, bcU1, bufA);
+
+  hipMemsetAsync(tiles, 0, 2097152, stream);
+  hipMemsetAsync(y1rec, 0, 26214400, stream);
   {
     const float* a0 = bufA;
     const unsigned short *w0 = wpU1Hi, *w1 = wpU1Lo, *w2 = wpU2Hi, *w3 = wpU2Lo;
     const float *b2 = bgU2, *c2 = bcU2;
-    unsigned *h1 = hPk1, *r1 = rPk1, *h2 = hPk2, *r2 = rPk2;
-    unsigned *s1p = bars + 256, *s2p = bars + 384;
-    unsigned short *yh = y1Hi, *yl = y1Lo;
+    u64 *h0 = hT0, *r0 = rT0, *yr = y1rec;
     float *op = out, *t1 = st1, *t2 = st2;
-    void* args[] = {&a0, &w0, &w1, &w2, &w3, &b2, &c2,
-                    &h1, &r1, &h2, &r2, &s1p, &s2p, &yh, &yl, &op, &t1, &t2};
+    void* args[] = {&a0, &w0, &w1, &w2, &w3, &b2, &c2, &h0, &r0, &yr, &op, &t1, &t2};
     hipLaunchCooperativeKernel((const void*)uni_fused_kernel, dim3(256), dim3(256),
                                args, 0, stream);
   }
```

Result: slower. 2.204 ms (+41.8%).
